# Kernel optimization log

Hardware: AMD Instinct MI355X
Metric: run time of the kernel (lower is better)

The kernel has to match this reference:

```python
import jax, jax.numpy as jnp
import numpy as np

B, S, HID = 4, 1024, 1024
NH = 16
DH = HID // NH  # 64


def _split_heads(t):
    # [B, S, HID] -> [B, NH, S, DH]
    return t.reshape(B, S, NH, DH).transpose(0, 2, 1, 3)


def _merge_heads(t):
    # [B, NH, S, DH] -> [B, S, HID]
    return t.transpose(0, 2, 1, 3).reshape(B, S, HID)


def setup_inputs() -> dict:
    key = jax.random.key(0)
    ks = jax.random.split(key, 13)
    scale = 1.0 / np.sqrt(HID)
    inp = {"x": jax.random.normal(ks[0], (B, S, HID), dtype=jnp.float32)}
    names = ["Wq", "Wk", "Wv", "Wq2", "Wk2", "Wv2"]
    for i, n in enumerate(names):
        inp[n] = jax.random.normal(ks[1 + i], (HID, HID), dtype=jnp.float32) * scale
        inp["b" + n[1:]] = jax.random.normal(ks[7 + i], (HID,), dtype=jnp.float32) * 0.01
    return inp


def _attn(q, k, v):
    # q,k,v: [B, NH, S, DH]
    scores = jnp.einsum("bhqd,bhkd->bhqk", q, k) / np.sqrt(DH).astype(np.float32)
    probs = jax.nn.softmax(scores, axis=-1)
    return jnp.einsum("bhqk,bhkd->bhqd", probs, v)


def reference(x, Wq, bq, Wk, bk, Wv, bv, Wq2, bq2, Wk2, bk2, Wv2, bv2):
    # nn.Linear: y = x @ W.T + b
    q1 = _split_heads(x @ Wq.T + bq)
    k1 = _split_heads(x @ Wk.T + bk)
    v1 = _split_heads(x @ Wv.T + bv)
    q2 = _split_heads(x @ Wq2.T + bq2)
    k2 = _split_heads(x @ Wk2.T + bk2)
    v2 = _split_heads(x @ Wv2.T + bv2)
    # 5'UTR direction: q1 attends to k2/v2; 3'UTR direction: q2 attends to k1/v1
    out5 = _merge_heads(_attn(q1, k2, v2))
    out3 = _merge_heads(_attn(q2, k1, v1))
    return (out5, out3)
```

## Files before the change

### kernel.cpp

```cpp
#include <hip/hip_runtime.h>


typedef __attribute__((ext_vector_type(8))) short bf16x8;
typedef __attribute__((ext_vector_type(4))) short bf16x4;
typedef __attribute__((ext_vector_type(4))) float f32x4;
typedef __attribute__((ext_vector_type(4))) short s16x4;

#define MFMA16(a, b, c) __builtin_amdgcn_mfma_f32_16x16x32_bf16(a, b, c, 0, 0, 0)

__device__ __forceinline__ f32x4 mfma16k(bf16x4 a, bf16x4 b, f32x4 c) {
#if __has_builtin(__builtin_amdgcn_mfma_f32_16x16x16bf16_1k)
  return __builtin_amdgcn_mfma_f32_16x16x16bf16_1k(a, b, c, 0, 0, 0);
#elif __has_builtin(__builtin_amdgcn_mfma_f32_16x16x16_bf16)
  return __builtin_amdgcn_mfma_f32_16x16x16_bf16(a, b, c, 0, 0, 0);
#else
  asm volatile("v_mfma_f32_16x16x16_bf16 %0, %1, %2, %0"
               : "+v"(c) : "v"(a), "v"(b));
  return c;
#endif
}

__device__ __forceinline__ unsigned short f2bf(float f) {
  unsigned u = __float_as_uint(f);
  u = (u + 0x7fffu + ((u >> 16) & 1u)) >> 16;
  return (unsigned short)u;
}

__device__ __forceinline__ unsigned cvt_pk_bf16(float lo, float hi) {
  unsigned r;
  asm("v_cvt_pk_bf16_f32 %0, %1, %2" : "=v"(r) : "v"(lo), "v"(hi));
  return r;
}

__device__ __forceinline__ void gll16(const void* g, void* l) {
  __builtin_amdgcn_global_load_lds(
      (const __attribute__((address_space(1))) unsigned int*)g,
      (__attribute__((address_space(3))) unsigned int*)l, 16, 0, 0);
}

__global__ __launch_bounds__(256) void convert_k(
    const float* __restrict__ x,
    const float* __restrict__ W0, const float* __restrict__ W1,
    const float* __restrict__ W2, const float* __restrict__ W3,
    const float* __restrict__ W4, const float* __restrict__ W5,
    short* __restrict__ xbf, short* __restrict__ wbf) {
  const int tid = blockIdx.x * 256 + threadIdx.x;
  const int e = tid << 2;
  const float* src;
  short* dst;
  int off;
  if (e < (4 << 20)) {
    src = x; dst = xbf; off = e;
  } else {
    const int j = e - (4 << 20);
    const int wsel = j >> 20;
    off = j & ((1 << 20) - 1);
    src = (wsel == 0) ? W0 : (wsel == 1) ? W1 : (wsel == 2) ? W2
        : (wsel == 3) ? W3 : (wsel == 4) ? W4 : W5;
    dst = wbf + ((size_t)wsel << 20);
  }
  const float4 v = *(const float4*)(src + off);
  s16x4 o;
  o.x = (short)f2bf(v.x);
  o.y = (short)f2bf(v.y);
  o.z = (short)f2bf(v.z);
  o.w = (short)f2bf(v.w);
  *(s16x4*)(dst + off) = o;
}

__global__ __launch_bounds__(256, 3) void proj_gemm32(
    const short* __restrict__ Ag, const short* __restrict__ W,
    const float* __restrict__ bq, const float* __restrict__ bk,
    const float* __restrict__ bv, const float* __restrict__ bq2,
    const float* __restrict__ bk2, const float* __restrict__ bv2,
    short* __restrict__ qkv) {
  __shared__ __align__(16) short As[3][128 * 32];
  __shared__ __align__(16) short Bs[3][128 * 32];

  const int bid = blockIdx.x;
  const int xcd = bid & 7, i = bid >> 3;
  const int nb = xcd * 6 + (i >> 5);
  const int mb = i & 31;
  const int p = nb >> 3;
  const int n0 = (nb & 7) << 7, m0 = mb << 7;

  const short* Bg = W + ((size_t)p << 20);
  const int t = threadIdx.x, lane = t & 63, w = t >> 6;
  const int g = lane >> 4, lr = lane & 15;
  const int wm = ((w >> 1) << 6), wn = ((w & 1) << 6);

  f32x4 acc[4][4] = {};

  auto stage = [&](int kt, int buf) {
    const int k0 = kt << 5;
#pragma unroll
    for (int ld = 0; ld < 2; ++ld) {
      const int slot = ld * 256 + t;
      const int rr = slot >> 2;
      const int gc = (slot & 3) ^ (rr & 3);
      gll16(Ag + (size_t)(m0 + rr) * 1024 + k0 + (gc << 3),
            &As[buf][slot * 8]);
      gll16(Bg + (size_t)(n0 + rr) * 1024 + k0 + (gc << 3),
            &Bs[buf][slot * 8]);
    }
  };

  stage(0, 0);
  stage(1, 1);
  asm volatile("s_waitcnt vmcnt(4)" ::: "memory");
  __builtin_amdgcn_s_barrier();

  int buf = 0;
  for (int T = 0; T < 32; ++T) {
    if (T <= 29) stage(T + 2, (T + 2) % 3);

    bf16x8 af[4], bfr[4];
#pragma unroll
    for (int mi = 0; mi < 4; ++mi) {
      const int rA = wm + mi * 16 + lr;
      af[mi] = *(const bf16x8*)&As[buf][rA * 32 + ((g ^ (rA & 3)) << 3)];
    }
#pragma unroll
    for (int nj = 0; nj < 4; ++nj) {
      const int rB = wn + nj * 16 + lr;
      bfr[nj] = *(const bf16x8*)&Bs[buf][rB * 32 + ((g ^ (rB & 3)) << 3)];
    }

    __builtin_amdgcn_s_setprio(1);
#pragma unroll
    for (int mi = 0; mi < 4; ++mi)
#pragma unroll
      for (int nj = 0; nj < 4; ++nj)
        acc[mi][nj] = MFMA16(af[mi], bfr[nj], acc[mi][nj]);
    __builtin_amdgcn_s_setprio(0);

    if (T <= 29) {
      asm volatile("s_waitcnt vmcnt(4)" ::: "memory");
    } else if (T == 30) {
      asm volatile("s_waitcnt vmcnt(0)" ::: "memory");
    }
    __builtin_amdgcn_s_barrier();
    buf = (buf == 2) ? 0 : buf + 1;
  }

  const float* bias = (p == 0) ? bq : (p == 1) ? bk : (p == 2) ? bv
                    : (p == 3) ? bq2 : (p == 4) ? bk2 : bv2;
  const int ptype = (p == 0 || p == 3) ? 0 : (p == 1 || p == 4) ? 1 : 2;
  unsigned short* dst = (unsigned short*)qkv + ((size_t)p << 22);
#pragma unroll
  for (int nj = 0; nj < 4; ++nj) {
    const int n = n0 + wn + nj * 16 + lr;
    const float bb = bias[n];
    const int h = n >> 6, d = n & 63;
#pragma unroll
    for (int mi = 0; mi < 4; ++mi) {
#pragma unroll
      for (int r = 0; r < 4; ++r) {
        const int m = m0 + wm + mi * 16 + (g << 2) + r;
        const int b = m >> 10, s = m & 1023;
        const unsigned short val = f2bf(acc[mi][nj][r] + bb);
        size_t idx;
        if (ptype == 0) {
          idx = ((size_t)(((b << 4) + h) * 1024 + s) << 6) + d;
        } else if (ptype == 1) {
          const int d2 = (d & 7) | (((d >> 3) ^ (s & 7)) << 3);
          idx = ((size_t)(((b << 4) + h) * 1024 + s) << 6) + d2;
        } else {
          const int tt = s >> 6, s2 = s & 63;
          const int s3 = (s2 & 7) | (((s2 >> 3) ^ (d & 7)) << 3);
          idx = ((size_t)((((b << 4) + h) * 16 + tt) * 64 + d) << 6) + s3;
        }
        dst[idx] = val;
      }
    }
  }
}

__global__ __launch_bounds__(256) void attn_k(const short* __restrict__ qkv,
                                              float* __restrict__ out) {
  __shared__ __align__(16) short Ks[2][64 * 64];
  __shared__ __align__(16) short Vs[2][64 * 64];

  const int L = blockIdx.x;
  const int xcd = L & 7, ss = L >> 3;
  const int qt = ss & 15, pg = ss >> 4;
  const int pp = xcd + (pg << 3);
  const int hb = pp & 63, dir = pp >> 6;

  const short* Q = qkv + ((size_t)(dir ? 3 : 0) << 22) + ((size_t)hb << 16);
  const short* K = qkv + ((size_t)(dir ? 1 : 4) << 22) + ((size_t)hb << 16);
  const short* V = qkv + ((size_t)(dir ? 2 : 5) << 22) + ((size_t)hb << 16);
  float* O = out + ((size_t)dir << 22);

  const int t = threadIdx.x, lane = t & 63, w = t >> 6;
  const int g = lane >> 4, lr = lane & 15;

  const int qrow = (qt << 6) + (w << 4) + lr;
  bf16x8 qf[2];
  qf[0] = *(const bf16x8*)(Q + qrow * 64 + g * 8);
  qf[1] = *(const bf16x8*)(Q + qrow * 64 + 32 + g * 8);

  const bf16x4 ones4 = {0x3F80, 0x3F80, 0x3F80, 0x3F80};

  f32x4 oacc[4] = {};
  f32x4 lacc = {};
  float mrun = -3.0e38f;
  const float CSC = 0.18033688f;

  const int srow = (w << 4) + (lane >> 3);
  const int scol = (lane & 7) << 3;

  auto stage = [&](int kt, int buf) {
#pragma unroll
    for (int i = 0; i < 2; ++i) {
      gll16(K + (size_t)((kt << 6) + srow + i * 8) * 64 + scol,
            &Ks[buf][(w << 10) + (i << 9)]);
      gll16(V + (size_t)(kt << 12) + (size_t)(srow + i * 8) * 64 + scol,
            &Vs[buf][(w << 10) + (i << 9)]);
    }
  };

  stage(0, 0);
  asm volatile("s_waitcnt vmcnt(0)" ::: "memory");
  __builtin_amdgcn_s_barrier();

  int cur = 0;
  for (int kt = 0; kt < 16; ++kt) {
    if (kt < 15) stage(kt + 1, cur ^ 1);

    f32x4 sc2[4] = {};
    __builtin_amdgcn_s_setprio(1);
#pragma unroll
    for (int dk = 0; dk < 2; ++dk) {
#pragma unroll
      for (int kn = 0; kn < 4; ++kn) {
        const int krow = kn * 16 + lr;
        const bf16x8 kf = *(const bf16x8*)
            &Ks[cur][krow * 64 +
                     ((((dk << 6) + (g << 4)) ^ ((krow & 7) << 4)) >> 1)];
        sc2[kn] = MFMA16(kf, qf[dk], sc2[kn]);
      }
    }
    __builtin_amdgcn_s_setprio(0);

    float tm = fmaxf(fmaxf(fmaxf(sc2[0][0], sc2[0][1]),
                           fmaxf(sc2[0][2], sc2[0][3])),
                     fmaxf(fmaxf(sc2[1][0], sc2[1][1]),
                           fmaxf(sc2[1][2], sc2[1][3])));
    tm = fmaxf(tm, fmaxf(fmaxf(fmaxf(sc2[2][0], sc2[2][1]),
                               fmaxf(sc2[2][2], sc2[2][3])),
                         fmaxf(fmaxf(sc2[3][0], sc2[3][1]),
                               fmaxf(sc2[3][2], sc2[3][3]))));
    const bool ok = __all(fmaf(tm, CSC, -mrun) <= 8.0f);
    if (!ok) {
      float t2 = fmaxf(tm, __shfl_xor(tm, 16));
      t2 = fmaxf(t2, __shfl_xor(t2, 32));
      const float mnew = fmaxf(mrun, t2 * CSC);
      const float scq = exp2f(mrun - mnew);
      mrun = mnew;
#pragma unroll
      for (int r = 0; r < 4; ++r) {
        const float sr = __shfl(scq, (g << 2) + r);
        lacc[r] *= sr;
#pragma unroll
        for (int dn = 0; dn < 4; ++dn) oacc[dn][r] *= sr;
      }
    }

    bf16x4 pa[4];
#pragma unroll
    for (int kn = 0; kn < 4; ++kn) {
      const float p0 = exp2f(fmaf(sc2[kn][0], CSC, -mrun));
      const float p1 = exp2f(fmaf(sc2[kn][1], CSC, -mrun));
      const float p2 = exp2f(fmaf(sc2[kn][2], CSC, -mrun));
      const float p3 = exp2f(fmaf(sc2[kn][3], CSC, -mrun));
      union { unsigned u[2]; bf16x4 v; } pk;
      pk.u[0] = cvt_pk_bf16(p0, p1);
      pk.u[1] = cvt_pk_bf16(p2, p3);
      pa[kn] = pk.v;
    }

    __builtin_amdgcn_s_setprio(1);
#pragma unroll
    for (int kn = 0; kn < 4; ++kn) {
      lacc = mfma16k(pa[kn], ones4, lacc);
#pragma unroll
      for (int dn = 0; dn < 4; ++dn) {
        const int vrow = dn * 16 + lr;
        const int ch = (2 * kn + (g >> 1)) ^ (vrow & 7);
        const bf16x4 vf = *(const bf16x4*)
            &Vs[cur][vrow * 64 + ch * 8 + ((g & 1) << 2)];
        oacc[dn] = mfma16k(pa[kn], vf, oacc[dn]);
      }
    }
    __builtin_amdgcn_s_setprio(0);

    asm volatile("s_waitcnt vmcnt(0)" ::: "memory");
    __builtin_amdgcn_s_barrier();
    cur ^= 1;
  }

  const int b = hb >> 4, h = hb & 15;
  float rl[4];
#pragma unroll
  for (int r = 0; r < 4; ++r) rl[r] = 1.0f / lacc[r];
#pragma unroll
  for (int dn = 0; dn < 4; ++dn) {
#pragma unroll
    for (int r = 0; r < 4; ++r) {
      const int q = (qt << 6) + (w << 4) + (g << 2) + r;
      const int d = dn * 16 + lr;
      O[((size_t)(b * 1024 + q) << 10) + h * 64 + d] = oacc[dn][r] * rl[r];
    }
  }
}

extern "C" void kernel_launch(void* const* d_in, const int* in_sizes, int n_in,
                              void* d_out, int out_size, void* d_ws,
                              size_t ws_size, hipStream_t stream) {
  const float* x   = (const float*)d_in[0];
  const float* Wq  = (const float*)d_in[1];
  const float* bq  = (const float*)d_in[2];
  const float* Wk  = (const float*)d_in[3];
  const float* bk  = (const float*)d_in[4];
  const float* Wv  = (const float*)d_in[5];
  const float* bv  = (const float*)d_in[6];
  const float* Wq2 = (const float*)d_in[7];
  const float* bq2 = (const float*)d_in[8];
  const float* Wk2 = (const float*)d_in[9];
  const float* bk2 = (const float*)d_in[10];
  const float* Wv2 = (const float*)d_in[11];
  const float* bv2 = (const float*)d_in[12];

  char* ws = (char*)d_ws;
  short* xbf = (short*)ws;
  short* wbf = (short*)(ws + 8388608);
  short* qkv = (short*)(ws + 20971520);

  convert_k<<<10240, 256, 0, stream>>>(x, Wq, Wk, Wv, Wq2, Wk2, Wv2, xbf, wbf);
  proj_gemm32<<<1536, 256, 0, stream>>>(xbf, wbf, bq, bk, bv, bq2, bk2,
                                        bv2, qkv);
  attn_k<<<2048, 256, 0, stream>>>(qkv, (float*)d_out);
}
```

Before: 170.1 us.

## Rewrite projection GEMM with 256x192 tiles, 512 threads and phased pipeline

The projection GEMM now uses 256x192 output tiles per 512-thread block, 64-wide K steps and double-buffered LDS, replacing 128x128 tiles, 32-wide K and triple buffering. Global-to-LDS loads are split into sub-stages interleaved between MFMA phases, separated by explicit barriers, in a ping-pong style schedule. The larger tile is meant to raise arithmetic intensity and cut redundant global loads, and it gives exactly 512 blocks for the 256-CU part. The cost is more accumulator registers per wave, heavier LDS use and more barriers per K step.

Result: faster. 163.0 us (-4.1%).

```diff
diff --git a/kernel.cpp b/kernel.cpp
--- a/kernel.cpp
+++ b/kernel.cpp
@@ -7,6 +7,8 @@
 typedef __attribute__((ext_vector_type(4))) short s16x4;
 
 #define MFMA16(a, b, c) __builtin_amdgcn_mfma_f32_16x16x32_bf16(a, b, c, 0, 0, 0)
+#define BARRIER() asm volatile("s_barrier" ::: "memory")
+#define VMCNT0() asm volatile("s_waitcnt vmcnt(0)" ::: "memory")
 
 __device__ __forceinline__ f32x4 mfma16k(bf16x4 a, bf16x4 b, f32x4 c) {
 #if __has_builtin(__builtin_amdgcn_mfma_f32_16x16x16bf16_1k)
@@ -68,109 +70,144 @@
   *(s16x4*)(dst + off) = o;
 }
 
-__global__ __launch_bounds__(256, 3) void proj_gemm32(
-    const short* __restrict__ Ag, const short* __restrict__ W,
+__global__ __launch_bounds__(512, 2) void proj_gemm192(
+    const short* __restrict__ Ag, const short* __restrict__ Wall,
     const float* __restrict__ bq, const float* __restrict__ bk,
     const float* __restrict__ bv, const float* __restrict__ bq2,
     const float* __restrict__ bk2, const float* __restrict__ bv2,
     short* __restrict__ qkv) {
-  __shared__ __align__(16) short As[3][128 * 32];
-  __shared__ __align__(16) short Bs[3][128 * 32];
+  __shared__ __align__(16) short As[2][16384];
+  __shared__ __align__(16) short Bs[2][12288];
 
   const int bid = blockIdx.x;
-  const int xcd = bid & 7, i = bid >> 3;
-  const int nb = xcd * 6 + (i >> 5);
-  const int mb = i & 31;
-  const int p = nb >> 3;
-  const int n0 = (nb & 7) << 7, m0 = mb << 7;
-
-  const short* Bg = W + ((size_t)p << 20);
+  const int xcd = bid & 7, k = bid >> 3;
+  const int ns = k & 3, mb = k >> 2;
+  const int nbase = (xcd * 4 + ns) * 192;
+  const int m0 = mb << 8;
+
   const int t = threadIdx.x, lane = t & 63, w = t >> 6;
   const int g = lane >> 4, lr = lane & 15;
-  const int wm = ((w >> 1) << 6), wn = ((w & 1) << 6);
-
-  f32x4 acc[4][4] = {};
-
-  auto stage = [&](int kt, int buf) {
-    const int k0 = kt << 5;
+  const int wr = w >> 2, wc = w & 3;
+
+  f32x4 acc[2][4][3] = {};
+
+  auto stage_ah = [&](int T, int H) {
 #pragma unroll
     for (int ld = 0; ld < 2; ++ld) {
-      const int slot = ld * 256 + t;
-      const int rr = slot >> 2;
-      const int gc = (slot & 3) ^ (rr & 3);
-      gll16(Ag + (size_t)(m0 + rr) * 1024 + k0 + (gc << 3),
-            &As[buf][slot * 8]);
-      gll16(Bg + (size_t)(n0 + rr) * 1024 + k0 + (gc << 3),
-            &Bs[buf][slot * 8]);
+      const int slot = (H << 10) + (ld << 9) + t;
+      const int rr = slot >> 3;
+      const int gc = (slot & 7) ^ (rr & 7);
+      gll16(Ag + (size_t)(m0 + rr) * 1024 + (T << 6) + (gc << 3),
+            &As[T & 1][slot * 8]);
     }
   };
-
-  stage(0, 0);
-  stage(1, 1);
-  asm volatile("s_waitcnt vmcnt(4)" ::: "memory");
-  __builtin_amdgcn_s_barrier();
-
-  int buf = 0;
-  for (int T = 0; T < 32; ++T) {
-    if (T <= 29) stage(T + 2, (T + 2) % 3);
-
-    bf16x8 af[4], bfr[4];
-#pragma unroll
-    for (int mi = 0; mi < 4; ++mi) {
-      const int rA = wm + mi * 16 + lr;
-      af[mi] = *(const bf16x8*)&As[buf][rA * 32 + ((g ^ (rA & 3)) << 3)];
-    }
-#pragma unroll
-    for (int nj = 0; nj < 4; ++nj) {
-      const int rB = wn + nj * 16 + lr;
-      bfr[nj] = *(const bf16x8*)&Bs[buf][rB * 32 + ((g ^ (rB & 3)) << 3)];
-    }
-
-    __builtin_amdgcn_s_setprio(1);
-#pragma unroll
-    for (int mi = 0; mi < 4; ++mi)
-#pragma unroll
-      for (int nj = 0; nj < 4; ++nj)
-        acc[mi][nj] = MFMA16(af[mi], bfr[nj], acc[mi][nj]);
-    __builtin_amdgcn_s_setprio(0);
-
-    if (T <= 29) {
-      asm volatile("s_waitcnt vmcnt(4)" ::: "memory");
-    } else if (T == 30) {
-      asm volatile("s_waitcnt vmcnt(0)" ::: "memory");
-    }
-    __builtin_amdgcn_s_barrier();
-    buf = (buf == 2) ? 0 : buf + 1;
-  }
-
-  const float* bias = (p == 0) ? bq : (p == 1) ? bk : (p == 2) ? bv
+  auto stage_b = [&](int T) {
+#pragma unroll
+    for (int ld = 0; ld < 3; ++ld) {
+      const int slot = (ld << 9) + t;
+      const int rr = slot >> 3;
+      const int gc = (slot & 7) ^ (rr & 7);
+      gll16(Wall + (size_t)(nbase + rr) * 1024 + (T << 6) + (gc << 3),
+            &Bs[T & 1][slot * 8]);
+    }
+  };
+
+  stage_ah(0, 0); stage_ah(0, 1); stage_b(0);
+  VMCNT0();
+  BARRIER();
+
+#define LOAD_A(MH, KK, TB)                                                \
+  _Pragma("unroll") for (int mi = 0; mi < 4; ++mi) {                      \
+    const int rA = wr * 128 + (MH) * 64 + mi * 16 + lr;                   \
+    af[mi] = *(const bf16x8*)                                             \
+        &As[TB][rA * 64 + ((((KK) * 4 + g) ^ (rA & 7)) << 3)];            \
+  }
+#define LOAD_B(KK, TB)                                                    \
+  _Pragma("unroll") for (int nj = 0; nj < 3; ++nj) {                      \
+    const int rB = wc * 48 + nj * 16 + lr;                                \
+    bf[nj] = *(const bf16x8*)                                             \
+        &Bs[TB][rB * 64 + ((((KK) * 4 + g) ^ (rB & 7)) << 3)];            \
+  }
+#define MFMA_PH(MH)                                                       \
+  __builtin_amdgcn_s_setprio(1);                                          \
+  _Pragma("unroll") for (int mi = 0; mi < 4; ++mi)                        \
+    _Pragma("unroll") for (int nj = 0; nj < 3; ++nj)                      \
+      acc[MH][mi][nj] = MFMA16(af[mi], bf[nj], acc[MH][mi][nj]);          \
+  __builtin_amdgcn_s_setprio(0);
+
+  auto group = [&](int C, int TC, int TD, bool DV) {
+    bf16x8 af[4], bf[3];
+    {
+      LOAD_A(0, 0, C); LOAD_B(0, C);
+      if (DV) stage_ah(TD, 0);
+      BARRIER();
+      MFMA_PH(0);
+      BARRIER();
+    }
+    {
+      LOAD_A(1, 0, C);
+      if (DV) stage_ah(TD, 1);
+      BARRIER();
+      MFMA_PH(1);
+      BARRIER();
+    }
+    {
+      LOAD_A(0, 1, C); LOAD_B(1, C);
+      if (DV) stage_b(TD);
+      BARRIER();
+      MFMA_PH(0);
+      BARRIER();
+    }
+    {
+      LOAD_A(1, 1, C);
+      BARRIER();
+      MFMA_PH(1);
+      VMCNT0();
+      BARRIER();
+    }
+  };
+
+  for (int j = 0; j < 8; ++j) {
+    group(0, 2 * j, 2 * j + 1, true);
+    group(1, 2 * j + 1, 2 * j + 2, j < 7);
+  }
+
+#undef LOAD_A
+#undef LOAD_B
+#undef MFMA_PH
+
+#pragma unroll
+  for (int nj = 0; nj < 3; ++nj) {
+    const int nn = nbase + wc * 48 + nj * 16 + lr;
+    const int p = nn >> 10, nl = nn & 1023;
+    const float* bp = (p == 0) ? bq : (p == 1) ? bk : (p == 2) ? bv
                     : (p == 3) ? bq2 : (p == 4) ? bk2 : bv2;
-  const int ptype = (p == 0 || p == 3) ? 0 : (p == 1 || p == 4) ? 1 : 2;
-  unsigned short* dst = (unsigned short*)qkv + ((size_t)p << 22);
-#pragma unroll
-  for (int nj = 0; nj < 4; ++nj) {
-    const int n = n0 + wn + nj * 16 + lr;
-    const float bb = bias[n];
-    const int h = n >> 6, d = n & 63;
-#pragma unroll
-    for (int mi = 0; mi < 4; ++mi) {
-#pragma unroll
-      for (int r = 0; r < 4; ++r) {
-        const int m = m0 + wm + mi * 16 + (g << 2) + r;
-        const int b = m >> 10, s = m & 1023;
-        const unsigned short val = f2bf(acc[mi][nj][r] + bb);
-        size_t idx;
-        if (ptype == 0) {
-          idx = ((size_t)(((b << 4) + h) * 1024 + s) << 6) + d;
-        } else if (ptype == 1) {
-          const int d2 = (d & 7) | (((d >> 3) ^ (s & 7)) << 3);
-          idx = ((size_t)(((b << 4) + h) * 1024 + s) << 6) + d2;
-        } else {
-          const int tt = s >> 6, s2 = s & 63;
-          const int s3 = (s2 & 7) | (((s2 >> 3) ^ (d & 7)) << 3);
-          idx = ((size_t)((((b << 4) + h) * 16 + tt) * 64 + d) << 6) + s3;
+    const float bb = bp[nl];
+    const int h = nl >> 6, d = nl & 63;
+    const int pt = (p == 0 || p == 3) ? 0 : (p == 1 || p == 4) ? 1 : 2;
+    unsigned short* dst = (unsigned short*)qkv + ((size_t)p << 22);
+#pragma unroll
+    for (int mh = 0; mh < 2; ++mh) {
+#pragma unroll
+      for (int mi = 0; mi < 4; ++mi) {
+#pragma unroll
+        for (int r = 0; r < 4; ++r) {
+          const int m = m0 + wr * 128 + mh * 64 + mi * 16 + (g << 2) + r;
+          const int b = m >> 10, s = m & 1023;
+          const unsigned short val = f2bf(acc[mh][mi][nj][r] + bb);
+          size_t idx;
+          if (pt == 0) {
+            idx = ((size_t)(((b << 4) + h) * 1024 + s) << 6) + d;
+          } else if (pt == 1) {
+            const int d2 = (d & 7) | (((d >> 3) ^ (s & 7)) << 3);
+            idx = ((size_t)(((b << 4) + h) * 1024 + s) << 6) + d2;
+          } else {
+            const int tt = s >> 6, s2 = s & 63;
+            const int s3 = (s2 & 7) | (((s2 >> 3) ^ (d & 7)) << 3);
+            idx = ((size_t)((((b << 4) + h) * 16 + tt) * 64 + d) << 6) + s3;
+          }
+          dst[idx] = val;
         }
-        dst[idx] = val;
       }
     }
   }
@@ -221,8 +258,8 @@
   };
 
   stage(0, 0);
-  asm volatile("s_waitcnt vmcnt(0)" ::: "memory");
-  __builtin_amdgcn_s_barrier();
+  VMCNT0();
+  BARRIER();
 
   int cur = 0;
   for (int kt = 0; kt < 16; ++kt) {
@@ -295,8 +332,8 @@
     }
     __builtin_amdgcn_s_setprio(0);
 
-    asm volatile("s_waitcnt vmcnt(0)" ::: "memory");
-    __builtin_amdgcn_s_barrier();
+    VMCNT0();
+    BARRIER();
     cur ^= 1;
   }
 
@@ -338,7 +375,7 @@
   short* qkv = (short*)(ws + 20971520);
 
   convert_k<<<10240, 256, 0, stream>>>(x, Wq, Wk, Wv, Wq2, Wk2, Wv2, xbf, wbf);
-  proj_gemm32<<<1536, 256, 0, stream>>>(xbf, wbf, bq, bk, bv, bq2, bk2,
+  proj_gemm192<<<512, 512, 0, stream>>>(xbf, wbf, bq, bk, bv, bq2, bk2,
                                         bv2, qkv);
   attn_k<<<2048, 256, 0, stream>>>(qkv, (float*)d_out);
 }
```

## Use 256x256 projection tiles with 32x32 MFMA and fragment double-buffering

Applied to the files above, without the earlier changes.

Rewrites the projection GEMM to use 256x256 output tiles per 512-thread block, with 32x32x16 bf16 MFMAs instead of 16x16x32. Fragment loads for the next half of each K-slice are issued before the MFMAs of the current half to overlap LDS reads with compute. Larger tiles raise operand reuse and cut global and LDS traffic per flop. The trade-off is fewer blocks (384), so the grid fills the machine only about one wave deep, plus higher register and LDS pressure. Any N-tile now spans only one weight matrix, so bias and layout are chosen per column.

New measurement: 217.5 us. +27.9%, slower.

```diff
diff --git a/kernel.cpp b/kernel.cpp
--- a/kernel.cpp
+++ b/kernel.cpp
@@ -4,9 +4,22 @@
 typedef __attribute__((ext_vector_type(8))) short bf16x8;
 typedef __attribute__((ext_vector_type(4))) short bf16x4;
 typedef __attribute__((ext_vector_type(4))) float f32x4;
+typedef __attribute__((ext_vector_type(16))) float f32x16;
 typedef __attribute__((ext_vector_type(4))) short s16x4;
 
 #define MFMA16(a, b, c) __builtin_amdgcn_mfma_f32_16x16x32_bf16(a, b, c, 0, 0, 0)
+#define BARRIER() asm volatile("s_barrier" ::: "memory")
+#define VMCNT0() asm volatile("s_waitcnt vmcnt(0)" ::: "memory")
+
+__device__ __forceinline__ f32x16 mfma32(bf16x8 a, bf16x8 b, f32x16 c) {
+#if __has_builtin(__builtin_amdgcn_mfma_f32_32x32x16_bf16)
+  return __builtin_amdgcn_mfma_f32_32x32x16_bf16(a, b, c, 0, 0, 0);
+#else
+  asm volatile("v_mfma_f32_32x32x16_bf16 %0, %1, %2, %0"
+               : "+v"(c) : "v"(a), "v"(b));
+  return c;
+#endif
+}
 
 __device__ __forceinline__ f32x4 mfma16k(bf16x4 a, bf16x4 b, f32x4 c) {
 #if __has_builtin(__builtin_amdgcn_mfma_f32_16x16x16bf16_1k)
@@ -68,101 +81,114 @@
   *(s16x4*)(dst + off) = o;
 }
 
-__global__ __launch_bounds__(256, 3) void proj_gemm32(
-    const short* __restrict__ Ag, const short* __restrict__ W,
+__global__ __launch_bounds__(512, 2) void proj_gemm256(
+    const short* __restrict__ Ag, const short* __restrict__ Wall,
     const float* __restrict__ bq, const float* __restrict__ bk,
     const float* __restrict__ bv, const float* __restrict__ bq2,
     const float* __restrict__ bk2, const float* __restrict__ bv2,
     short* __restrict__ qkv) {
-  __shared__ __align__(16) short As[3][128 * 32];
-  __shared__ __align__(16) short Bs[3][128 * 32];
+  __shared__ __align__(16) short As[3][8192];
+  __shared__ __align__(16) short Bs[3][8192];
 
   const int bid = blockIdx.x;
   const int xcd = bid & 7, i = bid >> 3;
-  const int nb = xcd * 6 + (i >> 5);
-  const int mb = i & 31;
-  const int p = nb >> 3;
-  const int n0 = (nb & 7) << 7, m0 = mb << 7;
-
-  const short* Bg = W + ((size_t)p << 20);
+  const int nb = xcd * 3 + (i >> 4);
+  const int mb = i & 15;
+  const int n0 = nb << 8, m0 = mb << 8;
+
   const int t = threadIdx.x, lane = t & 63, w = t >> 6;
-  const int g = lane >> 4, lr = lane & 15;
-  const int wm = ((w >> 1) << 6), wn = ((w & 1) << 6);
-
-  f32x4 acc[4][4] = {};
-
-  auto stage = [&](int kt, int buf) {
-    const int k0 = kt << 5;
+  const int hi = lane >> 5, lo = lane & 31;
+  const int wr = w >> 2, wc = w & 3;
+
+  f32x16 acc[4][2] = {};
+  bf16x8 a0[4], b0[2], a1[4], b1[2];
+
+  auto stage = [&](int T, int buf) {
+    const int k0 = T << 5;
 #pragma unroll
     for (int ld = 0; ld < 2; ++ld) {
-      const int slot = ld * 256 + t;
+      const int slot = (ld << 9) + t;
       const int rr = slot >> 2;
       const int gc = (slot & 3) ^ (rr & 3);
       gll16(Ag + (size_t)(m0 + rr) * 1024 + k0 + (gc << 3),
             &As[buf][slot * 8]);
-      gll16(Bg + (size_t)(n0 + rr) * 1024 + k0 + (gc << 3),
+      gll16(Wall + (size_t)(n0 + rr) * 1024 + k0 + (gc << 3),
             &Bs[buf][slot * 8]);
     }
   };
+
+#define LDFRAG(AV, BV, TB, KS)                                            \
+  _Pragma("unroll") for (int mi = 0; mi < 4; ++mi) {                      \
+    const int rA = wr * 128 + mi * 32 + lo;                               \
+    AV[mi] = *(const bf16x8*)                                             \
+        &As[TB][rA * 32 + (((((KS) << 1) + hi) ^ (rA & 3)) << 3)];        \
+  }                                                                       \
+  _Pragma("unroll") for (int nj = 0; nj < 2; ++nj) {                      \
+    const int rB = wc * 64 + nj * 32 + lo;                                \
+    BV[nj] = *(const bf16x8*)                                             \
+        &Bs[TB][rB * 32 + (((((KS) << 1) + hi) ^ (rB & 3)) << 3)];        \
+  }
+
+#define MFMA_C(AV, BV)                                                    \
+  __builtin_amdgcn_s_setprio(1);                                          \
+  _Pragma("unroll") for (int mi = 0; mi < 4; ++mi)                        \
+    _Pragma("unroll") for (int nj = 0; nj < 2; ++nj)                      \
+      acc[mi][nj] = mfma32(AV[mi], BV[nj], acc[mi][nj]);                  \
+  __builtin_amdgcn_s_setprio(0);
 
   stage(0, 0);
   stage(1, 1);
   asm volatile("s_waitcnt vmcnt(4)" ::: "memory");
-  __builtin_amdgcn_s_barrier();
-
-  int buf = 0;
+  BARRIER();
+  LDFRAG(a0, b0, 0, 0);
+
+  int bufT = 0;
   for (int T = 0; T < 32; ++T) {
-    if (T <= 29) stage(T + 2, (T + 2) % 3);
-
-    bf16x8 af[4], bfr[4];
+    const int bufN = (bufT == 2) ? 0 : bufT + 1;
+    const int bufS = (bufN == 2) ? 0 : bufN + 1;
+    if (T < 30) stage(T + 2, bufS);
+    LDFRAG(a1, b1, bufT, 1);
+    __builtin_amdgcn_sched_barrier(0);
+    MFMA_C(a0, b0);
+    if (T < 31) {
+      if (T < 30) {
+        asm volatile("s_waitcnt vmcnt(4)" ::: "memory");
+      } else {
+        VMCNT0();
+      }
+      BARRIER();
+      LDFRAG(a0, b0, bufN, 0);
+      __builtin_amdgcn_sched_barrier(0);
+    }
+    MFMA_C(a1, b1);
+    bufT = bufN;
+  }
+
+#undef LDFRAG
+#undef MFMA_C
+
+#pragma unroll
+  for (int nj = 0; nj < 2; ++nj) {
+    const int nn = n0 + wc * 64 + nj * 32 + lo;
+    const int p = nn >> 10, nl = nn & 1023;
+    const float* bp = (p == 0) ? bq : (p == 1) ? bk : (p == 2) ? bv
+                    : (p == 3) ? bq2 : (p == 4) ? bk2 : bv2;
+    const float bb = bp[nl];
+    const int h = nl >> 6, d = nl & 63;
+    const int pt = (p == 0 || p == 3) ? 0 : (p == 1 || p == 4) ? 1 : 2;
+    unsigned short* dst = (unsigned short*)qkv + ((size_t)p << 22);
 #pragma unroll
     for (int mi = 0; mi < 4; ++mi) {
-      const int rA = wm + mi * 16 + lr;
-      af[mi] = *(const bf16x8*)&As[buf][rA * 32 + ((g ^ (rA & 3)) << 3)];
-    }
-#pragma unroll
-    for (int nj = 0; nj < 4; ++nj) {
-      const int rB = wn + nj * 16 + lr;
-      bfr[nj] = *(const bf16x8*)&Bs[buf][rB * 32 + ((g ^ (rB & 3)) << 3)];
-    }
-
-    __builtin_amdgcn_s_setprio(1);
-#pragma unroll
-    for (int mi = 0; mi < 4; ++mi)
-#pragma unroll
-      for (int nj = 0; nj < 4; ++nj)
-        acc[mi][nj] = MFMA16(af[mi], bfr[nj], acc[mi][nj]);
-    __builtin_amdgcn_s_setprio(0);
-
-    if (T <= 29) {
-      asm volatile("s_waitcnt vmcnt(4)" ::: "memory");
-    } else if (T == 30) {
-      asm volatile("s_waitcnt vmcnt(0)" ::: "memory");
-    }
-    __builtin_amdgcn_s_barrier();
-    buf = (buf == 2) ? 0 : buf + 1;
-  }
-
-  const float* bias = (p == 0) ? bq : (p == 1) ? bk : (p == 2) ? bv
-                    : (p == 3) ? bq2 : (p == 4) ? bk2 : bv2;
-  const int ptype = (p == 0 || p == 3) ? 0 : (p == 1 || p == 4) ? 1 : 2;
-  unsigned short* dst = (unsigned short*)qkv + ((size_t)p << 22);
-#pragma unroll
-  for (int nj = 0; nj < 4; ++nj) {
-    const int n = n0 + wn + nj * 16 + lr;
-    const float bb = bias[n];
-    const int h = n >> 6, d = n & 63;
-#pragma unroll
-    for (int mi = 0; mi < 4; ++mi) {
-#pragma unroll
-      for (int r = 0; r < 4; ++r) {
-        const int m = m0 + wm + mi * 16 + (g << 2) + r;
+#pragma unroll
+      for (int r = 0; r < 16; ++r) {
+        const int m = m0 + wr * 128 + mi * 32 + (r & 3) + ((r >> 2) << 3) +
+                      (hi << 2);
         const int b = m >> 10, s = m & 1023;
         const unsigned short val = f2bf(acc[mi][nj][r] + bb);
         size_t idx;
-        if (ptype == 0) {
+        if (pt == 0) {
           idx = ((size_t)(((b << 4) + h) * 1024 + s) << 6) + d;
-        } else if (ptype == 1) {
+        } else if (pt == 1) {
           const int d2 = (d & 7) | (((d >> 3) ^ (s & 7)) << 3);
           idx = ((size_t)(((b << 4) + h) * 1024 + s) << 6) + d2;
         } else {
@@ -221,8 +247,8 @@
   };
 
   stage(0, 0);
-  asm volatile("s_waitcnt vmcnt(0)" ::: "memory");
-  __builtin_amdgcn_s_barrier();
+  VMCNT0();
+  BARRIER();
 
   int cur = 0;
   for (int kt = 0; kt < 16; ++kt) {
@@ -295,8 +321,8 @@
     }
     __builtin_amdgcn_s_setprio(0);
 
-    asm volatile("s_waitcnt vmcnt(0)" ::: "memory");
-    __builtin_amdgcn_s_barrier();
+    VMCNT0();
+    BARRIER();
     cur ^= 1;
   }
 
@@ -338,7 +364,7 @@
   short* qkv = (short*)(ws + 20971520);
 
   convert_k<<<10240, 256, 0, stream>>>(x, Wq, Wk, Wv, Wq2, Wk2, Wv2, xbf, wbf);
-  proj_gemm32<<<1536, 256, 0, stream>>>(xbf, wbf, bq, bk, bv, bq2, bk2,
+  proj_gemm256<<<384, 512, 0, stream>>>(xbf, wbf, bq, bk, bv, bq2, bk2,
                                         bv2, qkv);
   attn_k<<<2048, 256, 0, stream>>>(qkv, (float*)d_out);
 }
```
